# Kernel tuning notes

Hardware: AMD Instinct MI355X
Metric: run time of the kernel (lower is better)

The kernel has to match this reference:

```python
import jax, jax.numpy as jnp
import numpy as np

HEADS = 16
DIM_HEAD = 64
DIM = 1024
INNER = HEADS * DIM_HEAD  # 1024


def setup_inputs() -> dict:
    key = jax.random.key(0)
    ks = jax.random.split(key, 8)
    B, N, M = 4, 2048, 2048
    x = jax.random.normal(ks[0], (B, N, DIM), dtype=jnp.float32)
    context = jax.random.normal(ks[1], (B, M, DIM), dtype=jnp.float32)
    x_mask = (jax.random.uniform(ks[2], (B, N)) > 0.1).astype(jnp.float32)
    context_mask = (jax.random.uniform(ks[3], (B, M)) > 0.1).astype(jnp.float32)
    s = 0.02
    Wq = jax.random.normal(ks[4], (DIM, INNER), dtype=jnp.float32) * s
    Wkv = jax.random.normal(ks[5], (DIM, 2 * INNER), dtype=jnp.float32) * s
    Wo = jax.random.normal(ks[6], (INNER, DIM), dtype=jnp.float32) * s
    bo = jnp.zeros((DIM,), dtype=jnp.float32)
    return {"x": x, "context": context, "x_mask": x_mask,
            "context_mask": context_mask, "Wq": Wq, "Wkv": Wkv, "Wo": Wo, "bo": bo}


def _split_heads(t):
    b, n, _ = t.shape
    return t.reshape(b, n, HEADS, DIM_HEAD).transpose(0, 2, 1, 3)  # b h n d


def reference(x, context, x_mask, context_mask, Wq, Wkv, Wo, bo):
    scale = DIM_HEAD ** -0.5
    q = _split_heads(x @ Wq)                       # b h n d
    kv = context @ Wkv
    k = _split_heads(kv[..., :INNER])              # b h m d
    v = _split_heads(kv[..., INNER:])              # b h m d
    dots = jnp.einsum('bhnd,bhmd->bhnm', q, k) * scale
    # attn_bias = 1 - x_mask ⊗ context_mask; masked where isclose(attn_bias, 1)
    prod = x_mask[:, None, :, None] * context_mask[:, None, None, :]  # b 1 n m
    masked = jnp.isclose(1.0 - prod, 1.0)          # b 1 n m, broadcast over heads
    dots = jnp.where(masked, -jnp.inf, dots)       # b h n m
    # rows with no valid key: zero the whole row before softmax
    valid = jnp.any(~masked, axis=-1, keepdims=True)  # b 1 n 1
    dots = jnp.where(valid, dots, 0.0)
    attn = jax.nn.softmax(dots, axis=-1)
    attn = jnp.where(valid, attn, 0.0)
    out = jnp.einsum('bhnm,bhmd->bhnd', attn, v)
    b, h, n, d = out.shape
    out = out.transpose(0, 2, 1, 3).reshape(b, n, h * d)
    return out @ Wo + bo
```

## Files before the change

### kernel.cpp

```cpp
#include <hip/hip_runtime.h>

#define DEVI __device__ __forceinline__

typedef __attribute__((ext_vector_type(4))) float f32x4;
typedef __attribute__((ext_vector_type(8))) _Float16 f16x8;
typedef __attribute__((ext_vector_type(2))) _Float16 f16x2;

#if __has_builtin(__builtin_amdgcn_exp2f)
#define EXP2F __builtin_amdgcn_exp2f
#else
#define EXP2F exp2f
#endif

DEVI ushort f2h(float f) {
  _Float16 h = (_Float16)f;
  return __builtin_bit_cast(ushort, h);
}

DEVI unsigned pkrtz(float a, float b) {
  return __builtin_bit_cast(unsigned, __builtin_amdgcn_cvt_pkrtz(a, b));
}

DEVI float dot2acc(unsigned pk, float acc) {
#if __has_builtin(__builtin_amdgcn_fdot2)
  f16x2 one2 = {(_Float16)1.0f, (_Float16)1.0f};
  return __builtin_amdgcn_fdot2(__builtin_bit_cast(f16x2, pk), one2, acc, false);
#else
  f16x2 v = __builtin_bit_cast(f16x2, pk);
  return acc + (float)v[0] + (float)v[1];
#endif
}

DEVI void gload_lds16(const void* g, void* l) {
  typedef const unsigned int GlobU __attribute__((address_space(1)));
  typedef unsigned int LdsU __attribute__((address_space(3)));
  __builtin_amdgcn_global_load_lds((GlobU*)g, (LdsU*)l, 16, 0, 0);
}

__global__ __launch_bounds__(256) void cast_f16_kernel(
    const float4* __restrict__ x, const float4* __restrict__ ctx,
    ushort4* __restrict__ xo, ushort4* __restrict__ co) {
  int i = blockIdx.x * 256 + threadIdx.x;
  const float4* src;
  ushort4* dst;
  int j;
  if (i < 2097152) { src = x; dst = xo; j = i; }
  else             { src = ctx; dst = co; j = i - 2097152; }
  float4 v = src[j];
  ushort4 o;
  o.x = f2h(v.x); o.y = f2h(v.y); o.z = f2h(v.z); o.w = f2h(v.w);
  dst[j] = o;
}

__global__ __launch_bounds__(256) void transpose_cast_kernel(
    const float* __restrict__ Wq, const float* __restrict__ Wkv,
    const float* __restrict__ Wo, ushort* __restrict__ WqT,
    ushort* __restrict__ WkvT, ushort* __restrict__ WoT) {
  __shared__ ushort tile[64][65];
  int bx = blockIdx.x;
  const float* in; ushort* out; int C, cb;
  if (bx < 16)      { in = Wq;  out = WqT;  C = 1024; cb = bx * 64; }
  else if (bx < 48) { in = Wkv; out = WkvT; C = 2048; cb = (bx - 16) * 64; }
  else              { in = Wo;  out = WoT;  C = 1024; cb = (bx - 48) * 64; }
  const int R = 1024;
  int rb = blockIdx.y * 64;
  int t = threadIdx.x;
  int c4 = (t & 15) * 4, r0 = t >> 4;
#pragma unroll
  for (int i = 0; i < 4; i++) {
    int r = r0 + i * 16;
    float4 v = *(const float4*)(in + (size_t)(rb + r) * C + cb + c4);
    tile[r][c4 + 0] = f2h(v.x);
    tile[r][c4 + 1] = f2h(v.y);
    tile[r][c4 + 2] = f2h(v.z);
    tile[r][c4 + 3] = f2h(v.w);
  }
  __syncthreads();
#pragma unroll
  for (int i = 0; i < 4; i++) {
    int rr = r0 + i * 16;
    ushort4 o;
    o.x = tile[c4 + 0][rr]; o.y = tile[c4 + 1][rr];
    o.z = tile[c4 + 2][rr]; o.w = tile[c4 + 3][rr];
    *(ushort4*)(out + (size_t)(cb + rr) * R + rb + c4) = o;
  }
}

DEVI void gemm_core(const ushort* __restrict__ A, const ushort* __restrict__ Bt,
                    int K, int rowbase, int colbase, int tid,
                    ushort* As, ushort* Bs, f32x4 acc[4][4]) {
  const int lane = tid & 63, wave = tid >> 6;
  const int quad = lane >> 4, ln = lane & 15;
  const int wrow = (wave >> 1) * 64, wcol = (wave & 1) * 64;
  for (int k0 = 0; k0 < K; k0 += 32) {
    __syncthreads();
#pragma unroll
    for (int i = 0; i < 2; i++) {
      int f = i * 256 + tid;
      int r = f >> 2;
      int c = (f & 3) ^ (r & 3);
      gload_lds16(A + (size_t)(rowbase + r) * K + (k0 + c * 8),
                  (char*)As + (size_t)(i * 256 + wave * 64) * 16);
      gload_lds16(Bt + (size_t)(colbase + r) * K + (k0 + c * 8),
                  (char*)Bs + (size_t)(i * 256 + wave * 64) * 16);
    }
    __syncthreads();
    f16x8 a[4], b[4];
#pragma unroll
    for (int mt = 0; mt < 4; mt++) {
      int r = wrow + mt * 16 + ln;
      a[mt] = *(const f16x8*)(As + ((size_t)r * 4 + (quad ^ (r & 3))) * 8);
    }
#pragma unroll
    for (int nt = 0; nt < 4; nt++) {
      int r = wcol + nt * 16 + ln;
      b[nt] = *(const f16x8*)(Bs + ((size_t)r * 4 + (quad ^ (r & 3))) * 8);
    }
#pragma unroll
    for (int mt = 0; mt < 4; mt++)
#pragma unroll
      for (int nt = 0; nt < 4; nt++)
        acc[mt][nt] = __builtin_amdgcn_mfma_f32_16x16x32_f16(a[mt], b[nt], acc[mt][nt], 0, 0, 0);
  }
}

__global__ __launch_bounds__(256, 2) void qkv_gemm(
    const ushort* __restrict__ xb, const ushort* __restrict__ cb,
    const ushort* __restrict__ WqT, const ushort* __restrict__ WkvT,
    ushort* __restrict__ Qo, ushort* __restrict__ Ko, ushort* __restrict__ Vo) {
  __shared__ ushort As[128 * 32];
  __shared__ ushort Bs[128 * 32];
  const int tid = threadIdx.x;
  const int lane = tid & 63, wave = tid >> 6;
  const int quad = lane >> 4, ln = lane & 15;
  const int bx = blockIdx.x;
  const bool isQ = bx < 8;
  const int colbase = (isQ ? bx : bx - 8) * 128;
  const int rowbase = blockIdx.y * 128;
  const int wrow = (wave >> 1) * 64, wcol = (wave & 1) * 64;
  f32x4 acc[4][4] = {};
  gemm_core(isQ ? xb : cb, isQ ? WqT : WkvT, 1024, rowbase, colbase, tid, As, Bs, acc);

  if (isQ) {
    const float qscale = 0.18033688011112042f;
#pragma unroll
    for (int nt = 0; nt < 4; nt++) {
      int col = colbase + wcol + nt * 16 + ln;
      int h = col >> 6, d = col & 63;
#pragma unroll
      for (int mt = 0; mt < 4; mt++) {
        int row = rowbase + wrow + mt * 16 + quad * 4;
#pragma unroll
        for (int r = 0; r < 4; r++) {
          int rr = row + r;
          int bb = rr >> 11, n = rr & 2047;
          Qo[(((size_t)bb * 16 + h) * 2048 + n) * 64 + d] = f2h(acc[mt][nt][r] * qscale);
        }
      }
    }
  } else {
    bool isK = (colbase < 1024);
#pragma unroll
    for (int nt = 0; nt < 4; nt++) {
      int col = colbase + wcol + nt * 16 + ln;
#pragma unroll
      for (int mt = 0; mt < 4; mt++) {
        int row = rowbase + wrow + mt * 16 + quad * 4;
        int bb = row >> 11, m = row & 2047;
        if (isK) {
          int h = col >> 6, d = col & 63;
#pragma unroll
          for (int r = 0; r < 4; r++)
            Ko[(((size_t)bb * 16 + h) * 2048 + (m + r)) * 64 + d] = f2h(acc[mt][nt][r]);
        } else {
          int c2 = col - 1024;
          int h = c2 >> 6, d = c2 & 63;
          uint2 pv;
          pv.x = pkrtz(acc[mt][nt][0], acc[mt][nt][1]);
          pv.y = pkrtz(acc[mt][nt][2], acc[mt][nt][3]);
          *(uint2*)(Vo + (((size_t)bb * 16 + h) * 64 + d) * 2048 + m) = pv;
        }
      }
    }
  }
}

__global__ __launch_bounds__(256, 2) void out_gemm(
    const ushort* __restrict__ A, const ushort* __restrict__ Bt,
    float* __restrict__ C, const float* __restrict__ bias) {
  __shared__ ushort As[128 * 32];
  __shared__ ushort Bs[128 * 32];
  const int tid = threadIdx.x;
  const int lane = tid & 63, wave = tid >> 6;
  const int quad = lane >> 4, ln = lane & 15;
  const int colbase = blockIdx.x * 128, rowbase = blockIdx.y * 128;
  const int wrow = (wave >> 1) * 64, wcol = (wave & 1) * 64;
  f32x4 acc[4][4] = {};
  gemm_core(A, Bt, 1024, rowbase, colbase, tid, As, Bs, acc);
#pragma unroll
  for (int nt = 0; nt < 4; nt++) {
    int col = colbase + wcol + nt * 16 + ln;
    float bv = bias[col];
#pragma unroll
    for (int mt = 0; mt < 4; mt++) {
      int row = rowbase + wrow + mt * 16 + quad * 4;
#pragma unroll
      for (int r = 0; r < 4; r++)
        C[(size_t)(row + r) * 1024 + col] = acc[mt][nt][r] + bv;
    }
  }
}

__global__ __launch_bounds__(256, 2) void attn_kernel(
    const ushort* __restrict__ Q, const ushort* __restrict__ K,
    const ushort* __restrict__ VT, const float* __restrict__ xmask,
    const float* __restrict__ cmask, ushort* __restrict__ O) {
  __shared__ ushort Ks[2][64 * 64];
  __shared__ ushort Vs[2][64 * 64];
  __shared__ ushort Ps[4 * 64 * 40];
  __shared__ float CMB[2048];
  const int tid = threadIdx.x, lane = tid & 63, wave = tid >> 6;
  const int quad = lane >> 4, ln = lane & 15;
  const int bid = blockIdx.x;
  const int qb = bid & 7, h = (bid >> 3) & 15, b = bid >> 7;
  const size_t bh = (size_t)b * 16 + h;
  const ushort* Qbh = Q + bh * (2048 * 64);
  const ushort* Kbh = K + bh * (2048 * 64);
  const ushort* Vbh = VT + bh * (64 * 2048);
  const int q0 = qb * 256 + wave * 64;

  {
    float4 c0 = *(const float4*)(cmask + b * 2048 + tid * 8);
    float4 c1 = *(const float4*)(cmask + b * 2048 + tid * 8 + 4);
    float4 b0, b1;
    b0.x = fmaf(c0.x, 3.0e4f, -3.0e4f); b0.y = fmaf(c0.y, 3.0e4f, -3.0e4f);
    b0.z = fmaf(c0.z, 3.0e4f, -3.0e4f); b0.w = fmaf(c0.w, 3.0e4f, -3.0e4f);
    b1.x = fmaf(c1.x, 3.0e4f, -3.0e4f); b1.y = fmaf(c1.y, 3.0e4f, -3.0e4f);
    b1.z = fmaf(c1.z, 3.0e4f, -3.0e4f); b1.w = fmaf(c1.w, 3.0e4f, -3.0e4f);
    *(float4*)(CMB + tid * 8) = b0;
    *(float4*)(CMB + tid * 8 + 4) = b1;
  }

  f16x8 qf[4][2];
#pragma unroll
  for (int qt = 0; qt < 4; qt++)
#pragma unroll
    for (int kc = 0; kc < 2; kc++)
      qf[qt][kc] = *(const f16x8*)(Qbh + (size_t)(q0 + qt * 16 + ln) * 64 + kc * 32 + quad * 8);

  float xm[4];
#pragma unroll
  for (int qt = 0; qt < 4; qt++) xm[qt] = xmask[b * 2048 + q0 + qt * 16 + ln];

  __syncthreads();

#pragma unroll
  for (int t = 0; t < 2; t++) {
#pragma unroll
    for (int i = 0; i < 2; i++) {
      int f = i * 256 + tid;
      int r = f >> 3;
      int c = (f & 7) ^ (r & 7);
      gload_lds16(Kbh + (size_t)(t * 64 + r) * 64 + c * 8,
                  (char*)Ks[t] + (size_t)(i * 256 + wave * 64) * 16);
      gload_lds16(Vbh + (size_t)r * 2048 + (t * 64 + c * 8),
                  (char*)Vs[t] + (size_t)(i * 256 + wave * 64) * 16);
    }
  }

  f32x4 o[4][4] = {};
  float lrun[4] = {0.f, 0.f, 0.f, 0.f};

  for (int kb = 0; kb < 32; kb++) {
    const int cur = kb & 1;
    const int m0 = kb * 64;
    const ushort* KsC = Ks[cur];
    const ushort* VsC = Vs[cur];

    if (kb < 31) asm volatile("s_waitcnt vmcnt(4)" ::: "memory");
    else         asm volatile("s_waitcnt vmcnt(0)" ::: "memory");
    asm volatile("s_barrier" ::: "memory");

    f32x4 bias4[4];
#pragma unroll
    for (int kt = 0; kt < 4; kt++)
      bias4[kt] = *(const f32x4*)(CMB + m0 + kt * 16 + quad * 4);

    f32x4 s[4][4];
#pragma unroll
    for (int kt = 0; kt < 4; kt++)
#pragma unroll
      for (int qt = 0; qt < 4; qt++) s[kt][qt] = bias4[kt];
#pragma unroll
    for (int kc = 0; kc < 2; kc++) {
#pragma unroll
      for (int kt = 0; kt < 4; kt++) {
        int r = kt * 16 + ln;
        f16x8 ka = *(const f16x8*)(KsC + ((size_t)r * 8 + ((kc * 4 + quad) ^ (r & 7))) * 8);
#pragma unroll
        for (int qt = 0; qt < 4; qt++)
          s[kt][qt] = __builtin_amdgcn_mfma_f32_16x16x32_f16(ka, qf[qt][kc], s[kt][qt], 0, 0, 0);
      }
    }

    float rs[4] = {0.f, 0.f, 0.f, 0.f};
#pragma unroll
    for (int kc = 0; kc < 2; kc++) {
#pragma unroll
      for (int qt = 0; qt < 4; qt++) {
        int qrow = qt * 16 + ln;
        ushort* pb = Ps + wave * (64 * 40) + qrow * 40;
#pragma unroll
        for (int t = 0; t < 2; t++) {
          int kt = kc * 2 + t;
          float p0 = EXP2F(s[kt][qt][0]);
          float p1 = EXP2F(s[kt][qt][1]);
          float p2 = EXP2F(s[kt][qt][2]);
          float p3 = EXP2F(s[kt][qt][3]);
          uint2 pv;
          pv.x = pkrtz(p0, p1);
          pv.y = pkrtz(p2, p3);
          rs[qt] = dot2acc(pv.x, rs[qt]);
          rs[qt] = dot2acc(pv.y, rs[qt]);
          *(uint2*)(pb + (t * 4 + quad) * 4) = pv;
        }
      }
      f16x8 pf[4];
#pragma unroll
      for (int qt = 0; qt < 4; qt++) {
        int qrow = qt * 16 + ln;
        pf[qt] = *(const f16x8*)(Ps + wave * (64 * 40) + qrow * 40 + quad * 8);
      }
#pragma unroll
      for (int dt = 0; dt < 4; dt++) {
        int r = dt * 16 + ln;
        f16x8 va = *(const f16x8*)(VsC + ((size_t)r * 8 + ((kc * 4 + quad) ^ (r & 7))) * 8);
#pragma unroll
        for (int qt = 0; qt < 4; qt++)
          o[dt][qt] = __builtin_amdgcn_mfma_f32_16x16x32_f16(va, pf[qt], o[dt][qt], 0, 0, 0);
      }
    }
#pragma unroll
    for (int qt = 0; qt < 4; qt++) {
      float r2 = rs[qt];
      r2 += __shfl_xor(r2, 16, 64);
      r2 += __shfl_xor(r2, 32, 64);
      lrun[qt] += r2;
    }

    asm volatile("s_barrier" ::: "memory");
    if (kb < 30) {
      const int m2 = m0 + 128;
#pragma unroll
      for (int i = 0; i < 2; i++) {
        int f = i * 256 + tid;
        int r = f >> 3;
        int c = (f & 7) ^ (r & 7);
        gload_lds16(Kbh + (size_t)(m2 + r) * 64 + c * 8,
                    (char*)Ks[cur] + (size_t)(i * 256 + wave * 64) * 16);
        gload_lds16(Vbh + (size_t)r * 2048 + (m2 + c * 8),
                    (char*)Vs[cur] + (size_t)(i * 256 + wave * 64) * 16);
      }
    }
  }

#pragma unroll
  for (int qt = 0; qt < 4; qt++) {
    float inv = (xm[qt] != 0.f && lrun[qt] > 0.f) ? (1.f / lrun[qt]) : 0.f;
    int n = q0 + qt * 16 + ln;
    ushort* ob = O + ((size_t)(b * 2048 + n) * 16 + h) * 64;
#pragma unroll
    for (int dt = 0; dt < 4; dt++) {
      uint2 pv;
      pv.x = pkrtz(o[dt][qt][0] * inv, o[dt][qt][1] * inv);
      pv.y = pkrtz(o[dt][qt][2] * inv, o[dt][qt][3] * inv);
      *(uint2*)(ob + dt * 16 + quad * 4) = pv;
    }
  }
}

extern "C" void kernel_launch(void* const* d_in, const int* in_sizes, int n_in,
                              void* d_out, int out_size, void* d_ws, size_t ws_size,
                              hipStream_t stream) {
  const float* x   = (const float*)d_in[0];
  const float* ctx = (const float*)d_in[1];
  const float* xm  = (const float*)d_in[2];
  const float* cm  = (const float*)d_in[3];
  const float* Wq  = (const float*)d_in[4];
  const float* Wkv = (const float*)d_in[5];
  const float* Wo  = (const float*)d_in[6];
  const float* bo  = (const float*)d_in[7];

  char* ws = (char*)d_ws;
  const size_t MB = 1024 * 1024;
  ushort* xb   = (ushort*)(ws + 0);
  ushort* cb   = (ushort*)(ws + 16 * MB);
  ushort* WqT  = (ushort*)(ws + 32 * MB);
  ushort* WkvT = (ushort*)(ws + 34 * MB);
  ushort* WoT  = (ushort*)(ws + 38 * MB);
  ushort* Qb   = (ushort*)(ws + 40 * MB);
  ushort* Kb   = (ushort*)(ws + 56 * MB);
  ushort* VTb  = (ushort*)(ws + 72 * MB);
  ushort* Ob   = xb;

  cast_f16_kernel<<<16384, 256, 0, stream>>>((const float4*)x, (const float4*)ctx,
                                             (ushort4*)xb, (ushort4*)cb);
  transpose_cast_kernel<<<dim3(64, 16), 256, 0, stream>>>(Wq, Wkv, Wo, WqT, WkvT, WoT);
  qkv_gemm<<<dim3(24, 64), 256, 0, stream>>>(xb, cb, WqT, WkvT, Qb, Kb, VTb);
  attn_kernel<<<512, 256, 0, stream>>>(Qb, Kb, VTb, xm, cm, Ob);
  out_gemm<<<dim3(8, 64), 256, 0, stream>>>(Ob, WoT, (float*)d_out, bo);
}
```

Measured before the change: 320.7 us.

## Use 8-wave attention blocks with 32 query rows per wave and transpose GEMM grids

After: 313.4 us. 1.02x faster.

```diff
diff --git a/kernel.cpp b/kernel.cpp
--- a/kernel.cpp
+++ b/kernel.cpp
@@ -133,10 +133,10 @@
   const int tid = threadIdx.x;
   const int lane = tid & 63, wave = tid >> 6;
   const int quad = lane >> 4, ln = lane & 15;
-  const int bx = blockIdx.x;
-  const bool isQ = bx < 8;
-  const int colbase = (isQ ? bx : bx - 8) * 128;
-  const int rowbase = blockIdx.y * 128;
+  const int cy = blockIdx.y;
+  const bool isQ = cy < 8;
+  const int colbase = (isQ ? cy : cy - 8) * 128;
+  const int rowbase = blockIdx.x * 128;
   const int wrow = (wave >> 1) * 64, wcol = (wave & 1) * 64;
   f32x4 acc[4][4] = {};
   gemm_core(isQ ? xb : cb, isQ ? WqT : WkvT, 1024, rowbase, colbase, tid, As, Bs, acc);
@@ -193,7 +193,7 @@
   const int tid = threadIdx.x;
   const int lane = tid & 63, wave = tid >> 6;
   const int quad = lane >> 4, ln = lane & 15;
-  const int colbase = blockIdx.x * 128, rowbase = blockIdx.y * 128;
+  const int colbase = blockIdx.y * 128, rowbase = blockIdx.x * 128;
   const int wrow = (wave >> 1) * 64, wcol = (wave & 1) * 64;
   f32x4 acc[4][4] = {};
   gemm_core(A, Bt, 1024, rowbase, colbase, tid, As, Bs, acc);
@@ -211,65 +211,57 @@
   }
 }
 
-__global__ __launch_bounds__(256, 2) void attn_kernel(
+__global__ __launch_bounds__(512, 4) void attn_kernel(
     const ushort* __restrict__ Q, const ushort* __restrict__ K,
     const ushort* __restrict__ VT, const float* __restrict__ xmask,
     const float* __restrict__ cmask, ushort* __restrict__ O) {
   __shared__ ushort Ks[2][64 * 64];
   __shared__ ushort Vs[2][64 * 64];
-  __shared__ ushort Ps[4 * 64 * 40];
+  __shared__ ushort Ps[8 * 32 * 40];
   __shared__ float CMB[2048];
   const int tid = threadIdx.x, lane = tid & 63, wave = tid >> 6;
   const int quad = lane >> 4, ln = lane & 15;
   const int bid = blockIdx.x;
-  const int qb = bid & 7, h = (bid >> 3) & 15, b = bid >> 7;
+  const int qb = bid >> 6, bh6 = bid & 63, h = bh6 & 15, b = bh6 >> 4;
   const size_t bh = (size_t)b * 16 + h;
   const ushort* Qbh = Q + bh * (2048 * 64);
   const ushort* Kbh = K + bh * (2048 * 64);
   const ushort* Vbh = VT + bh * (64 * 2048);
-  const int q0 = qb * 256 + wave * 64;
+  const int q0 = qb * 256 + wave * 32;
 
   {
-    float4 c0 = *(const float4*)(cmask + b * 2048 + tid * 8);
-    float4 c1 = *(const float4*)(cmask + b * 2048 + tid * 8 + 4);
-    float4 b0, b1;
+    float4 c0 = *(const float4*)(cmask + b * 2048 + tid * 4);
+    float4 b0;
     b0.x = fmaf(c0.x, 3.0e4f, -3.0e4f); b0.y = fmaf(c0.y, 3.0e4f, -3.0e4f);
     b0.z = fmaf(c0.z, 3.0e4f, -3.0e4f); b0.w = fmaf(c0.w, 3.0e4f, -3.0e4f);
-    b1.x = fmaf(c1.x, 3.0e4f, -3.0e4f); b1.y = fmaf(c1.y, 3.0e4f, -3.0e4f);
-    b1.z = fmaf(c1.z, 3.0e4f, -3.0e4f); b1.w = fmaf(c1.w, 3.0e4f, -3.0e4f);
-    *(float4*)(CMB + tid * 8) = b0;
-    *(float4*)(CMB + tid * 8 + 4) = b1;
-  }
-
-  f16x8 qf[4][2];
-#pragma unroll
-  for (int qt = 0; qt < 4; qt++)
+    *(float4*)(CMB + tid * 4) = b0;
+  }
+
+  f16x8 qf[2][2];
+#pragma unroll
+  for (int qt = 0; qt < 2; qt++)
 #pragma unroll
     for (int kc = 0; kc < 2; kc++)
       qf[qt][kc] = *(const f16x8*)(Qbh + (size_t)(q0 + qt * 16 + ln) * 64 + kc * 32 + quad * 8);
 
-  float xm[4];
-#pragma unroll
-  for (int qt = 0; qt < 4; qt++) xm[qt] = xmask[b * 2048 + q0 + qt * 16 + ln];
+  float xm[2];
+#pragma unroll
+  for (int qt = 0; qt < 2; qt++) xm[qt] = xmask[b * 2048 + q0 + qt * 16 + ln];
 
   __syncthreads();
 
-#pragma unroll
-  for (int t = 0; t < 2; t++) {
-#pragma unroll
-    for (int i = 0; i < 2; i++) {
-      int f = i * 256 + tid;
-      int r = f >> 3;
-      int c = (f & 7) ^ (r & 7);
-      gload_lds16(Kbh + (size_t)(t * 64 + r) * 64 + c * 8,
-                  (char*)Ks[t] + (size_t)(i * 256 + wave * 64) * 16);
-      gload_lds16(Vbh + (size_t)r * 2048 + (t * 64 + c * 8),
-                  (char*)Vs[t] + (size_t)(i * 256 + wave * 64) * 16);
-    }
-  }
-
-  f32x4 o[4][4] = {};
-  float lrun[4] = {0.f, 0.f, 0.f, 0.f};
+  {
+    int r = tid >> 3;
+    int c = (tid & 7) ^ (r & 7);
+#pragma unroll
+    for (int t = 0; t < 2; t++) {
+      gload_lds16(Kbh + (size_t)(t * 64 + r) * 64 + c * 8, (char*)Ks[t] + (size_t)tid * 16);
+      gload_lds16(Vbh + (size_t)r * 2048 + (t * 64 + c * 8), (char*)Vs[t] + (size_t)tid * 16);
+    }
+  }
+
+  f32x4 o[4][2] = {};
+  float lpart[2] = {0.f, 0.f};
 
   for (int kb = 0; kb < 32; kb++) {
     const int cur = kb & 1;
@@ -277,7 +269,7 @@
     const ushort* KsC = Ks[cur];
     const ushort* VsC = Vs[cur];
 
-    if (kb < 31) asm volatile("s_waitcnt vmcnt(4)" ::: "memory");
+    if (kb < 31) asm volatile("s_waitcnt vmcnt(2)" ::: "memory");
     else         asm volatile("s_waitcnt vmcnt(0)" ::: "memory");
     asm volatile("s_barrier" ::: "memory");
 
@@ -286,11 +278,11 @@
     for (int kt = 0; kt < 4; kt++)
       bias4[kt] = *(const f32x4*)(CMB + m0 + kt * 16 + quad * 4);
 
-    f32x4 s[4][4];
+    f32x4 s[4][2];
 #pragma unroll
     for (int kt = 0; kt < 4; kt++)
 #pragma unroll
-      for (int qt = 0; qt < 4; qt++) s[kt][qt] = bias4[kt];
+      for (int qt = 0; qt < 2; qt++) s[kt][qt] = bias4[kt];
 #pragma unroll
     for (int kc = 0; kc < 2; kc++) {
 #pragma unroll
@@ -298,18 +290,17 @@
         int r = kt * 16 + ln;
         f16x8 ka = *(const f16x8*)(KsC + ((size_t)r * 8 + ((kc * 4 + quad) ^ (r & 7))) * 8);
 #pragma unroll
-        for (int qt = 0; qt < 4; qt++)
+        for (int qt = 0; qt < 2; qt++)
           s[kt][qt] = __builtin_amdgcn_mfma_f32_16x16x32_f16(ka, qf[qt][kc], s[kt][qt], 0, 0, 0);
       }
     }
 
-    float rs[4] = {0.f, 0.f, 0.f, 0.f};
 #pragma unroll
     for (int kc = 0; kc < 2; kc++) {
 #pragma unroll
-      for (int qt = 0; qt < 4; qt++) {
+      for (int qt = 0; qt < 2; qt++) {
         int qrow = qt * 16 + ln;
-        ushort* pb = Ps + wave * (64 * 40) + qrow * 40;
+        ushort* pb = Ps + wave * (32 * 40) + qrow * 40;
 #pragma unroll
         for (int t = 0; t < 2; t++) {
           int kt = kc * 2 + t;
@@ -320,53 +311,43 @@
           uint2 pv;
           pv.x = pkrtz(p0, p1);
           pv.y = pkrtz(p2, p3);
-          rs[qt] = dot2acc(pv.x, rs[qt]);
-          rs[qt] = dot2acc(pv.y, rs[qt]);
+          lpart[qt] = dot2acc(pv.x, lpart[qt]);
+          lpart[qt] = dot2acc(pv.y, lpart[qt]);
           *(uint2*)(pb + (t * 4 + quad) * 4) = pv;
         }
       }
-      f16x8 pf[4];
-#pragma unroll
-      for (int qt = 0; qt < 4; qt++) {
+      f16x8 pf[2];
+#pragma unroll
+      for (int qt = 0; qt < 2; qt++) {
         int qrow = qt * 16 + ln;
-        pf[qt] = *(const f16x8*)(Ps + wave * (64 * 40) + qrow * 40 + quad * 8);
+        pf[qt] = *(const f16x8*)(Ps + wave * (32 * 40) + qrow * 40 + quad * 8);
       }
 #pragma unroll
       for (int dt = 0; dt < 4; dt++) {
         int r = dt * 16 + ln;
         f16x8 va = *(const f16x8*)(VsC + ((size_t)r * 8 + ((kc * 4 + quad) ^ (r & 7))) * 8);
 #pragma unroll
-        for (int qt = 0; qt < 4; qt++)
+        for (int qt = 0; qt < 2; qt++)
           o[dt][qt] = __builtin_amdgcn_mfma_f32_16x16x32_f16(va, pf[qt], o[dt][qt], 0, 0, 0);
       }
-    }
-#pragma unroll
-    for (int qt = 0; qt < 4; qt++) {
-      float r2 = rs[qt];
-      r2 += __shfl_xor(r2, 16, 64);
-      r2 += __shfl_xor(r2, 32, 64);
-      lrun[qt] += r2;
     }
 
     asm volatile("s_barrier" ::: "memory");
     if (kb < 30) {
       const int m2 = m0 + 128;
-#pragma unroll
-      for (int i = 0; i < 2; i++) {
-        int f = i * 256 + tid;
-        int r = f >> 3;
-        int c = (f & 7) ^ (r & 7);
-        gload_lds16(Kbh + (size_t)(m2 + r) * 64 + c * 8,
-                    (char*)Ks[cur] + (size_t)(i * 256 + wave * 64) * 16);
-        gload_lds16(Vbh + (size_t)r * 2048 + (m2 + c * 8),
-                    (char*)Vs[cur] + (size_t)(i * 256 + wave * 64) * 16);
-      }
-    }
-  }
-
-#pragma unroll
-  for (int qt = 0; qt < 4; qt++) {
-    float inv = (xm[qt] != 0.f && lrun[qt] > 0.f) ? (1.f / lrun[qt]) : 0.f;
+      int r = tid >> 3;
+      int c = (tid & 7) ^ (r & 7);
+      gload_lds16(Kbh + (size_t)(m2 + r) * 64 + c * 8, (char*)Ks[cur] + (size_t)tid * 16);
+      gload_lds16(Vbh + (size_t)r * 2048 + (m2 + c * 8), (char*)Vs[cur] + (size_t)tid * 16);
+    }
+  }
+
+#pragma unroll
+  for (int qt = 0; qt < 2; qt++) {
+    float l = lpart[qt];
+    l += __shfl_xor(l, 16, 64);
+    l += __shfl_xor(l, 32, 64);
+    float inv = (xm[qt] != 0.f && l > 0.f) ? (1.f / l) : 0.f;
     int n = q0 + qt * 16 + ln;
     ushort* ob = O + ((size_t)(b * 2048 + n) * 16 + h) * 64;
 #pragma unroll
@@ -406,7 +387,7 @@
   cast_f16_kernel<<<16384, 256, 0, stream>>>((const float4*)x, (const float4*)ctx,
                                              (ushort4*)xb, (ushort4*)cb);
   transpose_cast_kernel<<<dim3(64, 16), 256, 0, stream>>>(Wq, Wkv, Wo, WqT, WkvT, WoT);
-  qkv_gemm<<<dim3(24, 64), 256, 0, stream>>>(xb, cb, WqT, WkvT, Qb, Kb, VTb);
-  attn_kernel<<<512, 256, 0, stream>>>(Qb, Kb, VTb, xm, cm, Ob);
-  out_gemm<<<dim3(8, 64), 256, 0, stream>>>(Ob, WoT, (float*)d_out, bo);
-}
+  qkv_gemm<<<dim3(64, 24), 256, 0, stream>>>(xb, cb, WqT, WkvT, Qb, Kb, VTb);
+  attn_kernel<<<512, 512, 0, stream>>>(Qb, Kb, VTb, xm, cm, Ob);
+  out_gemm<<<dim3(64, 8), 256, 0, stream>>>(Ob, WoT, (float*)d_out, bo);
+}
```
